# Performance work log

Hardware: AMD Instinct MI355X
Metric: run time of the kernel (lower is better)

The kernel has to match this reference:

```python
import jax, jax.numpy as jnp
import numpy as np

B, W, L, J, I, O = 512, 1024, 64, 8, 32, 128


def setup_inputs() -> dict:
    key = jax.random.key(0)
    ks = jax.random.split(key, 9)
    wm = jax.random.normal(ks[0], (B, W, L), dtype=jnp.float32)
    constants = jax.random.uniform(ks[1], (J, L), minval=-1.0, maxval=1.0, dtype=jnp.float32)
    gammas = jax.random.uniform(ks[2], (J, L), minval=0.0, maxval=1.0, dtype=jnp.float32)
    body_w = jax.random.normal(ks[3], (J, I, L), dtype=jnp.float32) / np.sqrt(L).astype(np.float32)
    body_b = jax.random.normal(ks[4], (J, I), dtype=jnp.float32) * 0.01
    slot_w = jax.random.normal(ks[5], (J, L * I, L), dtype=jnp.float32) / np.sqrt(L).astype(np.float32)
    slot_b = jax.random.normal(ks[6], (J, L * I), dtype=jnp.float32) * 0.01
    head_w = jax.random.normal(ks[7], (O, I), dtype=jnp.float32) / np.sqrt(I).astype(np.float32)
    head_b = jax.random.normal(ks[8], (O,), dtype=jnp.float32) * 0.01
    return {"working_memory": wm, "constants": constants, "gammas": gammas,
            "body_w": body_w, "body_b": body_b, "slot_w": slot_w, "slot_b": slot_b,
            "head_w": head_w, "head_b": head_b}


def reference(working_memory, constants, gammas, body_w, body_b, slot_w, slot_b, head_w, head_b):
    temperature = 1.0
    g = jnp.clip(gammas, 0.0, 1.0)            # (J,L), torch.clamp equivalent
    w1 = 1.0 - g                               # per-element weight (1-gamma)
    # match_scores[j,b,w] = sum_l w1[j,l] * (c[j,l] - wm[b,w,l])^2, expanded to
    # avoid materializing a (J,B,W,L) intermediate:
    A = jnp.sum(w1 * constants * constants, axis=1)                      # (J,)
    cross = jnp.einsum('jl,bwl->jbw', w1 * constants, working_memory)    # (J,B,W)
    quad = jnp.einsum('jl,bwl->jbw', w1, working_memory * working_memory)
    scores = A[:, None, None] - 2.0 * cross + quad                       # (J,B,W)
    attn = jax.nn.softmax(-scores / temperature, axis=-1)                # (J,B,W)
    best = jnp.einsum('jbw,bwl->jbl', attn, working_memory)              # (J,B,L)
    total_mq = jnp.sum(attn * scores, axis=-1).sum(axis=0)               # (B,)
    # body: per-premise Linear(L->I), scaled by mean clamped gamma
    captured = jnp.einsum('jbl,jil->jbi', best, body_w) + body_b[:, None, :]
    g_avg = g.mean(axis=1)                                               # (J,)
    captured_vars = jnp.einsum('j,jbi->bi', g_avg, captured)             # (B,I)
    # slot selector: per-premise Linear(L -> L*I), softmax over slots,
    # scatter best_props values into slots (the original inner l-loop).
    slot_logits = jnp.einsum('jbl,jkl->jbk', best, slot_w) + slot_b[:, None, :]
    slot_probs = jax.nn.softmax(slot_logits.reshape(J, -1, L, I), axis=-1)
    captured_vars = captured_vars + jnp.einsum('jbli,jbl->bi', slot_probs, best)
    output = captured_vars @ head_w.T + head_b                           # (B,O)
    confidence = jnp.exp(-total_mq)[:, None]                             # (B,1)
    return confidence * output
```

## Files before the change

### kernel.cpp

```cpp
#include <hip/hip_runtime.h>
#include <cstdint>
#include <cstddef>

#define B_ 512
#define W_ 1024
#define L_ 64
#define J_ 8
#define I_ 32
#define O_ 128


typedef const __attribute__((address_space(1))) void* gas_ptr;
typedef __attribute__((address_space(3))) void* las_ptr;

__global__ __launch_bounds__(64) void k0_prep(const float* __restrict__ constants,
    const float* __restrict__ gammas, float* __restrict__ wcg,
    float* __restrict__ w1g, float* __restrict__ Ag)
{
  const int l = threadIdx.x;
  #pragma unroll
  for (int j = 0; j < J_; ++j) {
    float g = gammas[j*L_ + l];
    g = fminf(fmaxf(g, 0.f), 1.f);
    float c = constants[j*L_ + l];
    float w1 = 1.f - g;
    w1g[j*L_ + l] = w1;
    wcg[j*L_ + l] = -2.f * w1 * c;
  }
  if (l < J_) {
    float a = 0.f;
    for (int c = 0; c < L_; ++c) {
      float g = gammas[l*L_ + c];
      g = fminf(fmaxf(g, 0.f), 1.f);
      float cc = constants[l*L_ + c];
      a += (1.f - g) * cc * cc;
    }
    Ag[l] = a;
  }
}

__global__ __launch_bounds__(256, 2) void k12_fused(const float* __restrict__ wm,
    const float* __restrict__ wcg, const float* __restrict__ w1g,
    const float* __restrict__ Ag, float* __restrict__ bpart, float* __restrict__ stats)
{
  __shared__ __align__(16) float xs[2][64 * 64];
  __shared__ __align__(16) float es[4][64 * 2];

  const int tid = threadIdx.x;
  const int b = blockIdx.x, h = blockIdx.y;
  const int lane = tid & 63;
  const int wvu = __builtin_amdgcn_readfirstlane(tid >> 6);
  const int j0  = wvu * 2;
  const int wm15 = lane & 15;
  const int cg = lane & 15, rs = lane >> 4;
  const int rl = lane >> 4, pcg = lane & 15;

  const float* wmb = wm + (size_t)b * (W_*L_) + (size_t)h * (512*L_);

  float acc0[4] = {0.f, 0.f, 0.f, 0.f};
  float acc1[4] = {0.f, 0.f, 0.f, 0.f};
  float esum[2] = {0.f, 0.f}, msum[2] = {0.f, 0.f}, m0v[2];

  auto stage = [&](const float* csrc, float* ldst) {
    #pragma unroll
    for (int k = 0; k < 4; ++k) {
      const int grow = wvu*16 + k*4 + rl;
      const int lcg  = pcg ^ (k*4 + rl);
      __builtin_amdgcn_global_load_lds(
          (gas_ptr)(csrc + grow*64 + lcg*4),
          (las_ptr)(ldst + (wvu*16 + k*4)*64), 16, 0, 0);
    }
  };

  stage(wmb, &xs[0][0]);
  asm volatile("s_waitcnt vmcnt(0)" ::: "memory");
  __builtin_amdgcn_s_barrier();

  for (int ch = 0; ch < 8; ++ch) {
    float* xb = &xs[ch & 1][0];

    if (ch < 7)
      stage(wmb + (ch+1) * (64*L_), &xs[(ch+1) & 1][0]);

    float a10 = 0.f, a11 = 0.f, a20 = 0.f, a21 = 0.f;
    #pragma unroll
    for (int c = 0; c < 16; ++c) {
      const int col = c ^ wm15;
      float4 x = *(const float4*)&xb[lane*64 + col*4];
      float4 xq;
      xq.x = x.x*x.x; xq.y = x.y*x.y; xq.z = x.z*x.z; xq.w = x.w*x.w;
      float4 wc0 = *(const float4*)(wcg + (j0  )*L_ + c*4);
      float4 wc1 = *(const float4*)(wcg + (j0+1)*L_ + c*4);
      float4 w10 = *(const float4*)(w1g + (j0  )*L_ + c*4);
      float4 w11 = *(const float4*)(w1g + (j0+1)*L_ + c*4);
      a10 = fmaf(wc0.x, x.x, a10); a10 = fmaf(wc0.y, x.y, a10);
      a10 = fmaf(wc0.z, x.z, a10); a10 = fmaf(wc0.w, x.w, a10);
      a11 = fmaf(wc1.x, x.x, a11); a11 = fmaf(wc1.y, x.y, a11);
      a11 = fmaf(wc1.z, x.z, a11); a11 = fmaf(wc1.w, x.w, a11);
      a20 = fmaf(w10.x, xq.x, a20); a20 = fmaf(w10.y, xq.y, a20);
      a20 = fmaf(w10.z, xq.z, a20); a20 = fmaf(w10.w, xq.w, a20);
      a21 = fmaf(w11.x, xq.x, a21); a21 = fmaf(w11.y, xq.y, a21);
      a21 = fmaf(w11.w, xq.w, a21); a21 = fmaf(w11.z, xq.z, a21);
    }
    float s0v = Ag[j0]   + a10 + a20;
    float s1v = Ag[j0+1] + a11 + a21;

    if (ch == 0) {
      float mn0 = s0v, mn1 = s1v;
      #pragma unroll
      for (int off = 1; off < 64; off <<= 1) {
        mn0 = fminf(mn0, __shfl_xor(mn0, off));
        mn1 = fminf(mn1, __shfl_xor(mn1, off));
      }
      m0v[0] = mn0; m0v[1] = mn1;
    }

    float e0 = __expf(m0v[0] - s0v);
    float e1 = __expf(m0v[1] - s1v);
    esum[0] += e0; msum[0] = fmaf(e0, s0v, msum[0]);
    esum[1] += e1; msum[1] = fmaf(e1, s1v, msum[1]);
    *(float2*)&es[wvu][lane*2] = make_float2(e0, e1);

    asm volatile("s_waitcnt lgkmcnt(0)" ::: "memory");

    #pragma unroll
    for (int it = 0; it < 16; it += 2) {
      const int w0 = rs*16 + it;
      float4 e4 = *(const float4*)&es[wvu][w0*2];
      float4 xA = *(const float4*)&xb[w0*64     + (cg ^ ( w0    & 15))*4];
      float4 xB = *(const float4*)&xb[(w0+1)*64 + (cg ^ ((w0+1) & 15))*4];
      acc0[0] = fmaf(e4.x, xA.x, acc0[0]); acc0[1] = fmaf(e4.x, xA.y, acc0[1]);
      acc0[2] = fmaf(e4.x, xA.z, acc0[2]); acc0[3] = fmaf(e4.x, xA.w, acc0[3]);
      acc1[0] = fmaf(e4.y, xA.x, acc1[0]); acc1[1] = fmaf(e4.y, xA.y, acc1[1]);
      acc1[2] = fmaf(e4.y, xA.z, acc1[2]); acc1[3] = fmaf(e4.y, xA.w, acc1[3]);
      acc0[0] = fmaf(e4.z, xB.x, acc0[0]); acc0[1] = fmaf(e4.z, xB.y, acc0[1]);
      acc0[2] = fmaf(e4.z, xB.z, acc0[2]); acc0[3] = fmaf(e4.z, xB.w, acc0[3]);
      acc1[0] = fmaf(e4.w, xB.x, acc1[0]); acc1[1] = fmaf(e4.w, xB.y, acc1[1]);
      acc1[2] = fmaf(e4.w, xB.z, acc1[2]); acc1[3] = fmaf(e4.w, xB.w, acc1[3]);
    }

    if (ch < 7) {
      asm volatile("s_waitcnt vmcnt(0) lgkmcnt(0)" ::: "memory");
      __builtin_amdgcn_s_barrier();
    }
  }

  #pragma unroll
  for (int u = 0; u < 2; ++u) {
    float e = esum[u], m = msum[u];
    #pragma unroll
    for (int off = 1; off < 64; off <<= 1) {
      e += __shfl_xor(e, off);
      m += __shfl_xor(m, off);
    }
    if (lane == 0) {
      float* st = stats + (((size_t)h*B_ + b)*J_ + (j0+u))*4;
      st[0] = m0v[u]; st[1] = e; st[2] = m;
    }
  }

  #pragma unroll
  for (int q = 0; q < 4; ++q) {
    acc0[q] += __shfl_xor(acc0[q], 16);
    acc0[q] += __shfl_xor(acc0[q], 32);
    acc1[q] += __shfl_xor(acc1[q], 16);
    acc1[q] += __shfl_xor(acc1[q], 32);
  }
  if (lane < 16) {
    float* bp0 = &bpart[(((size_t)h*J_ + j0    )*B_ + b)*L_ + cg*4];
    float* bp1 = &bpart[(((size_t)h*J_ + j0 + 1)*B_ + b)*L_ + cg*4];
    *(float4*)bp0 = make_float4(acc0[0], acc0[1], acc0[2], acc0[3]);
    *(float4*)bp1 = make_float4(acc1[0], acc1[1], acc1[2], acc1[3]);
  }
}

__global__ __launch_bounds__(128) void k2b_combine(const float* __restrict__ bpart,
    const float* __restrict__ stats, float* __restrict__ best, float* __restrict__ conf)
{
  __shared__ float mred[J_];
  const int b = blockIdx.x, tid = threadIdx.x;
  const int j = tid >> 4, q = tid & 15;
  const float* st0 = stats + ((size_t)b*J_ + j)*4;
  const float* st1 = stats + (((size_t)B_ + b)*J_ + j)*4;
  float m0a = st0[0], E0 = st0[1], M0 = st0[2];
  float m0b = st1[0], E1 = st1[1], M1 = st1[2];
  float M = fminf(m0a, m0b);
  float s0 = __expf(M - m0a), s1 = __expf(M - m0b);
  float E = s0*E0 + s1*E1;
  float inv = 1.f / E;
  float4 p0 = *(const float4*)&bpart[((size_t)j*B_ + b)*L_ + q*4];
  float4 p1 = *(const float4*)&bpart[(((size_t)J_ + j)*B_ + b)*L_ + q*4];
  float4 o;
  o.x = (s0*p0.x + s1*p1.x) * inv;
  o.y = (s0*p0.y + s1*p1.y) * inv;
  o.z = (s0*p0.z + s1*p1.z) * inv;
  o.w = (s0*p0.w + s1*p1.w) * inv;
  *(float4*)&best[((size_t)j*B_ + b)*L_ + q*4] = o;
  if (q == 0) mred[j] = (s0*M0 + s1*M1) * inv;
  __syncthreads();
  if (tid == 0) {
    float mq = 0.f;
    #pragma unroll
    for (int jj = 0; jj < J_; ++jj) mq += mred[jj];
    conf[b] = __expf(-mq);
  }
}

__global__ __launch_bounds__(256) void k3_slot(const float* __restrict__ slot_w,
    const float* __restrict__ slot_b, const float* __restrict__ best,
    float* __restrict__ partial)
{
  const int bx = blockIdx.y;
  const int j = bx >> 3, lg = bx & 7;
  const int bc = blockIdx.x;
  const int tid = threadIdx.x;
  const int wv = tid >> 6, lane = tid & 63;
  const int l2 = lane >> 5, i = lane & 31;
  const int l = lg*8 + wv*2 + l2;
  const int r = l*I_ + i;

  const float* swr = slot_w + ((size_t)j*(L_*I_) + r) * L_;
  float sw[L_];
  #pragma unroll
  for (int c = 0; c < 16; ++c) {
    float4 t = ((const float4*)swr)[c];
    sw[c*4+0] = t.x; sw[c*4+1] = t.y; sw[c*4+2] = t.z; sw[c*4+3] = t.w;
  }
  const float sb = slot_b[j*(L_*I_) + r];
  const float* bestj = best + (size_t)j * B_ * L_;
  float* pout = partial + (size_t)bx * (B_*I_);
  const int lidx = lg*8 + wv*2;

  for (int bi = 0; bi < 32; bi += 4) {
    const int b0 = bc*32 + bi;
    const float* bw[4];
    #pragma unroll
    for (int u = 0; u < 4; ++u) bw[u] = bestj + (size_t)(b0+u) * L_;
    float pa[4], pb[4];
    #pragma unroll
    for (int u = 0; u < 4; ++u) { pa[u] = sb; pb[u] = 0.f; }
    #pragma unroll
    for (int c = 0; c < L_; c += 2) {
      #pragma unroll
      for (int u = 0; u < 4; ++u) {
        pa[u] = fmaf(bw[u][c+0], sw[c+0], pa[u]);
        pb[u] = fmaf(bw[u][c+1], sw[c+1], pb[u]);
      }
    }
    float e[4], sm[4];
    #pragma unroll
    for (int u = 0; u < 4; ++u) { e[u] = __expf(pa[u] + pb[u]); sm[u] = e[u]; }
    #pragma unroll
    for (int mask = 16; mask; mask >>= 1)
      #pragma unroll
      for (int u = 0; u < 4; ++u) sm[u] += __shfl_xor(sm[u], mask);
    float cv[4];
    #pragma unroll
    for (int u = 0; u < 4; ++u) {
      float bv = l2 ? bw[u][lidx+1] : bw[u][lidx];
      cv[u] = (e[u] / sm[u]) * bv;
    }
    #pragma unroll
    for (int u = 0; u < 4; ++u) cv[u] += __shfl_xor(cv[u], 32);
    if (l2 == 0) {
      #pragma unroll
      for (int u = 0; u < 4; ++u)
        pout[(size_t)(b0+u)*I_ + i] = cv[u];
    }
  }
}

__global__ __launch_bounds__(128) void k4_head(const float* __restrict__ partial,
    const float* __restrict__ best, const float* __restrict__ gammas,
    const float* __restrict__ body_w, const float* __restrict__ body_b,
    const float* __restrict__ head_w, const float* __restrict__ head_b,
    const float* __restrict__ conf, float* __restrict__ out)
{
  __shared__ float gavg[J_];
  __shared__ float cvred[4][I_];
  __shared__ float cvf[I_];
  const int b = blockIdx.x, tid = threadIdx.x;
  const int i = tid & 31, q = tid >> 5;
  if (tid < J_) {
    float gsum = 0.f;
    for (int l = 0; l < L_; ++l) {
      float g = gammas[tid*L_ + l];
      gsum += fminf(fmaxf(g, 0.f), 1.f);
    }
    gavg[tid] = gsum * (1.f / L_);
  }
  __syncthreads();

  float acc = 0.f;
  for (int s = q; s < 64; s += 4)
    acc += partial[((size_t)s*B_ + b)*I_ + i];

  #pragma unroll
  for (int u = 0; u < 2; ++u) {
    const int j = q + u*4;
    const float* bwv  = best + ((size_t)j*B_ + b)*L_;
    const float* wrow = body_w + (size_t)(j*I_ + i)*L_;
    float d0 = body_b[j*I_ + i], d1 = 0.f, d2 = 0.f, d3 = 0.f;
    #pragma unroll
    for (int c = 0; c < L_; c += 4) {
      d0 = fmaf(bwv[c+0], wrow[c+0], d0);
      d1 = fmaf(bwv[c+1], wrow[c+1], d1);
      d2 = fmaf(bwv[c+2], wrow[c+2], d2);
      d3 = fmaf(bwv[c+3], wrow[c+3], d3);
    }
    acc = fmaf(gavg[j], (d0 + d1) + (d2 + d3), acc);
  }
  cvred[q][i] = acc;
  __syncthreads();
  if (tid < I_)
    cvf[i] = cvred[0][i] + cvred[1][i] + cvred[2][i] + cvred[3][i];
  __syncthreads();
  float oacc = head_b[tid];
  #pragma unroll
  for (int i2 = 0; i2 < I_; ++i2) oacc = fmaf(cvf[i2], head_w[tid*I_ + i2], oacc);
  out[(size_t)b*O_ + tid] = conf[b] * oacc;
}

extern "C" void kernel_launch(void* const* d_in, const int* in_sizes, int n_in,
                              void* d_out, int out_size, void* d_ws, size_t ws_size,
                              hipStream_t stream) {
  const float* wm        = (const float*)d_in[0];
  const float* constants = (const float*)d_in[1];
  const float* gammas    = (const float*)d_in[2];
  const float* body_w    = (const float*)d_in[3];
  const float* body_b    = (const float*)d_in[4];
  const float* slot_w    = (const float*)d_in[5];
  const float* slot_b    = (const float*)d_in[6];
  const float* head_w    = (const float*)d_in[7];
  const float* head_b    = (const float*)d_in[8];
  float* out = (float*)d_out;

  float* ws      = (float*)d_ws;
  float* wcg     = ws;
  float* w1g     = wcg + J_*L_;
  float* Ag      = w1g + J_*L_;
  float* best    = Ag + 16;
  float* conf    = best + (size_t)J_*B_*L_;
  float* partial = conf + B_;
  float* bpart   = partial + (size_t)64*B_*I_;
  float* stats   = bpart + (size_t)2*J_*B_*L_;

  hipLaunchKernelGGL(k0_prep, dim3(1), dim3(64), 0, stream,
                     constants, gammas, wcg, w1g, Ag);
  hipLaunchKernelGGL(k12_fused, dim3(B_, 2), dim3(256), 0, stream,
                     wm, wcg, w1g, Ag, bpart, stats);
  hipLaunchKernelGGL(k2b_combine, dim3(B_), dim3(128), 0, stream,
                     bpart, stats, best, conf);
  hipLaunchKernelGGL(k3_slot, dim3(16, 64), dim3(256), 0, stream,
                     slot_w, slot_b, best, partial);
  hipLaunchKernelGGL(k4_head, dim3(B_), dim3(128), 0, stream,
                     partial, best, gammas, body_w, body_b, head_w, head_b, conf, out);
}
```

Measured before the change: 282.9 us.

## Split attention W dimension into eight blocks, combine partial softmax results

The fused score/attention kernel now launches 8 blocks per batch row instead of 2. Each block handles one 64-row chunk of working memory, so the in-block double-buffered chunk loop goes away. The combine kernel merges 8 partial (min, expsum, weighted-sum) statistics and partial best vectors with rescaling. This aims to raise parallelism and hide load latency by running many blocks at once rather than software pipelining. The cost is more partial-output traffic and a heavier combine step.

```diff
diff --git a/kernel.cpp b/kernel.cpp
--- a/kernel.cpp
+++ b/kernel.cpp
@@ -8,6 +8,7 @@
 #define J_ 8
 #define I_ 32
 #define O_ 128
+#define H_ 8
 
 
 typedef const __attribute__((address_space(1))) void* gas_ptr;
@@ -43,7 +44,7 @@
     const float* __restrict__ wcg, const float* __restrict__ w1g,
     const float* __restrict__ Ag, float* __restrict__ bpart, float* __restrict__ stats)
 {
-  __shared__ __align__(16) float xs[2][64 * 64];
+  __shared__ __align__(16) float xs[64 * 64];
   __shared__ __align__(16) float es[4][64 * 2];
 
   const int tid = threadIdx.x;
@@ -55,107 +56,86 @@
   const int cg = lane & 15, rs = lane >> 4;
   const int rl = lane >> 4, pcg = lane & 15;
 
-  const float* wmb = wm + (size_t)b * (W_*L_) + (size_t)h * (512*L_);
+  const float* wmb = wm + (size_t)b * (W_*L_) + (size_t)h * (64*L_);
+
+  #pragma unroll
+  for (int k = 0; k < 4; ++k) {
+    const int grow = wvu*16 + k*4 + rl;
+    const int lcg  = pcg ^ (k*4 + rl);
+    __builtin_amdgcn_global_load_lds(
+        (gas_ptr)(wmb + grow*64 + lcg*4),
+        (las_ptr)&xs[(wvu*16 + k*4)*64], 16, 0, 0);
+  }
+  asm volatile("s_waitcnt vmcnt(0)" ::: "memory");
+  __builtin_amdgcn_s_barrier();
+
+  float a10 = 0.f, a11 = 0.f, a20 = 0.f, a21 = 0.f;
+  #pragma unroll
+  for (int c = 0; c < 16; ++c) {
+    const int col = c ^ wm15;
+    float4 x = *(const float4*)&xs[lane*64 + col*4];
+    float4 xq;
+    xq.x = x.x*x.x; xq.y = x.y*x.y; xq.z = x.z*x.z; xq.w = x.w*x.w;
+    float4 wc0 = *(const float4*)(wcg + (j0  )*L_ + c*4);
+    float4 wc1 = *(const float4*)(wcg + (j0+1)*L_ + c*4);
+    float4 w10 = *(const float4*)(w1g + (j0  )*L_ + c*4);
+    float4 w11 = *(const float4*)(w1g + (j0+1)*L_ + c*4);
+    a10 = fmaf(wc0.x, x.x, a10); a10 = fmaf(wc0.y, x.y, a10);
+    a10 = fmaf(wc0.z, x.z, a10); a10 = fmaf(wc0.w, x.w, a10);
+    a11 = fmaf(wc1.x, x.x, a11); a11 = fmaf(wc1.y, x.y, a11);
+    a11 = fmaf(wc1.z, x.z, a11); a11 = fmaf(wc1.w, x.w, a11);
+    a20 = fmaf(w10.x, xq.x, a20); a20 = fmaf(w10.y, xq.y, a20);
+    a20 = fmaf(w10.z, xq.z, a20); a20 = fmaf(w10.w, xq.w, a20);
+    a21 = fmaf(w11.x, xq.x, a21); a21 = fmaf(w11.y, xq.y, a21);
+    a21 = fmaf(w11.z, xq.z, a21); a21 = fmaf(w11.w, xq.w, a21);
+  }
+  float s0v = Ag[j0]   + a10 + a20;
+  float s1v = Ag[j0+1] + a11 + a21;
+
+  float mn0 = s0v, mn1 = s1v;
+  #pragma unroll
+  for (int off = 1; off < 64; off <<= 1) {
+    mn0 = fminf(mn0, __shfl_xor(mn0, off));
+    mn1 = fminf(mn1, __shfl_xor(mn1, off));
+  }
+
+  float e0 = __expf(mn0 - s0v);
+  float e1 = __expf(mn1 - s1v);
+  float esum0 = e0, esum1 = e1;
+  float msum0 = e0 * s0v, msum1 = e1 * s1v;
+  *(float2*)&es[wvu][lane*2] = make_float2(e0, e1);
+  asm volatile("s_waitcnt lgkmcnt(0)" ::: "memory");
 
   float acc0[4] = {0.f, 0.f, 0.f, 0.f};
   float acc1[4] = {0.f, 0.f, 0.f, 0.f};
-  float esum[2] = {0.f, 0.f}, msum[2] = {0.f, 0.f}, m0v[2];
-
-  auto stage = [&](const float* csrc, float* ldst) {
-    #pragma unroll
-    for (int k = 0; k < 4; ++k) {
-      const int grow = wvu*16 + k*4 + rl;
-      const int lcg  = pcg ^ (k*4 + rl);
-      __builtin_amdgcn_global_load_lds(
-          (gas_ptr)(csrc + grow*64 + lcg*4),
-          (las_ptr)(ldst + (wvu*16 + k*4)*64), 16, 0, 0);
-    }
-  };
-
-  stage(wmb, &xs[0][0]);
-  asm volatile("s_waitcnt vmcnt(0)" ::: "memory");
-  __builtin_amdgcn_s_barrier();
-
-  for (int ch = 0; ch < 8; ++ch) {
-    float* xb = &xs[ch & 1][0];
-
-    if (ch < 7)
-      stage(wmb + (ch+1) * (64*L_), &xs[(ch+1) & 1][0]);
-
-    float a10 = 0.f, a11 = 0.f, a20 = 0.f, a21 = 0.f;
-    #pragma unroll
-    for (int c = 0; c < 16; ++c) {
-      const int col = c ^ wm15;
-      float4 x = *(const float4*)&xb[lane*64 + col*4];
-      float4 xq;
-      xq.x = x.x*x.x; xq.y = x.y*x.y; xq.z = x.z*x.z; xq.w = x.w*x.w;
-      float4 wc0 = *(const float4*)(wcg + (j0  )*L_ + c*4);
-      float4 wc1 = *(const float4*)(wcg + (j0+1)*L_ + c*4);
-      float4 w10 = *(const float4*)(w1g + (j0  )*L_ + c*4);
-      float4 w11 = *(const float4*)(w1g + (j0+1)*L_ + c*4);
-      a10 = fmaf(wc0.x, x.x, a10); a10 = fmaf(wc0.y, x.y, a10);
-      a10 = fmaf(wc0.z, x.z, a10); a10 = fmaf(wc0.w, x.w, a10);
-      a11 = fmaf(wc1.x, x.x, a11); a11 = fmaf(wc1.y, x.y, a11);
-      a11 = fmaf(wc1.z, x.z, a11); a11 = fmaf(wc1.w, x.w, a11);
-      a20 = fmaf(w10.x, xq.x, a20); a20 = fmaf(w10.y, xq.y, a20);
-      a20 = fmaf(w10.z, xq.z, a20); a20 = fmaf(w10.w, xq.w, a20);
-      a21 = fmaf(w11.x, xq.x, a21); a21 = fmaf(w11.y, xq.y, a21);
-      a21 = fmaf(w11.w, xq.w, a21); a21 = fmaf(w11.z, xq.z, a21);
-    }
-    float s0v = Ag[j0]   + a10 + a20;
-    float s1v = Ag[j0+1] + a11 + a21;
-
-    if (ch == 0) {
-      float mn0 = s0v, mn1 = s1v;
-      #pragma unroll
-      for (int off = 1; off < 64; off <<= 1) {
-        mn0 = fminf(mn0, __shfl_xor(mn0, off));
-        mn1 = fminf(mn1, __shfl_xor(mn1, off));
-      }
-      m0v[0] = mn0; m0v[1] = mn1;
-    }
-
-    float e0 = __expf(m0v[0] - s0v);
-    float e1 = __expf(m0v[1] - s1v);
-    esum[0] += e0; msum[0] = fmaf(e0, s0v, msum[0]);
-    esum[1] += e1; msum[1] = fmaf(e1, s1v, msum[1]);
-    *(float2*)&es[wvu][lane*2] = make_float2(e0, e1);
-
-    asm volatile("s_waitcnt lgkmcnt(0)" ::: "memory");
-
-    #pragma unroll
-    for (int it = 0; it < 16; it += 2) {
-      const int w0 = rs*16 + it;
-      float4 e4 = *(const float4*)&es[wvu][w0*2];
-      float4 xA = *(const float4*)&xb[w0*64     + (cg ^ ( w0    & 15))*4];
-      float4 xB = *(const float4*)&xb[(w0+1)*64 + (cg ^ ((w0+1) & 15))*4];
-      acc0[0] = fmaf(e4.x, xA.x, acc0[0]); acc0[1] = fmaf(e4.x, xA.y, acc0[1]);
-      acc0[2] = fmaf(e4.x, xA.z, acc0[2]); acc0[3] = fmaf(e4.x, xA.w, acc0[3]);
-      acc1[0] = fmaf(e4.y, xA.x, acc1[0]); acc1[1] = fmaf(e4.y, xA.y, acc1[1]);
-      acc1[2] = fmaf(e4.y, xA.z, acc1[2]); acc1[3] = fmaf(e4.y, xA.w, acc1[3]);
-      acc0[0] = fmaf(e4.z, xB.x, acc0[0]); acc0[1] = fmaf(e4.z, xB.y, acc0[1]);
-      acc0[2] = fmaf(e4.z, xB.z, acc0[2]); acc0[3] = fmaf(e4.z, xB.w, acc0[3]);
-      acc1[0] = fmaf(e4.w, xB.x, acc1[0]); acc1[1] = fmaf(e4.w, xB.y, acc1[1]);
-      acc1[2] = fmaf(e4.w, xB.z, acc1[2]); acc1[3] = fmaf(e4.w, xB.w, acc1[3]);
-    }
-
-    if (ch < 7) {
-      asm volatile("s_waitcnt vmcnt(0) lgkmcnt(0)" ::: "memory");
-      __builtin_amdgcn_s_barrier();
-    }
-  }
-
-  #pragma unroll
-  for (int u = 0; u < 2; ++u) {
-    float e = esum[u], m = msum[u];
+  #pragma unroll
+  for (int it = 0; it < 16; it += 2) {
+    const int w0 = rs*16 + it;
+    float4 e4 = *(const float4*)&es[wvu][w0*2];
+    float4 xA = *(const float4*)&xs[w0*64     + (cg ^ ( w0    & 15))*4];
+    float4 xB = *(const float4*)&xs[(w0+1)*64 + (cg ^ ((w0+1) & 15))*4];
+    acc0[0] = fmaf(e4.x, xA.x, acc0[0]); acc0[1] = fmaf(e4.x, xA.y, acc0[1]);
+    acc0[2] = fmaf(e4.x, xA.z, acc0[2]); acc0[3] = fmaf(e4.x, xA.w, acc0[3]);
+    acc1[0] = fmaf(e4.y, xA.x, acc1[0]); acc1[1] = fmaf(e4.y, xA.y, acc1[1]);
+    acc1[2] = fmaf(e4.y, xA.z, acc1[2]); acc1[3] = fmaf(e4.y, xA.w, acc1[3]);
+    acc0[0] = fmaf(e4.z, xB.x, acc0[0]); acc0[1] = fmaf(e4.z, xB.y, acc0[1]);
+    acc0[2] = fmaf(e4.z, xB.z, acc0[2]); acc0[3] = fmaf(e4.z, xB.w, acc0[3]);
+    acc1[0] = fmaf(e4.w, xB.x, acc1[0]); acc1[1] = fmaf(e4.w, xB.y, acc1[1]);
+    acc1[2] = fmaf(e4.w, xB.z, acc1[2]); acc1[3] = fmaf(e4.w, xB.w, acc1[3]);
+  }
+
+  {
+    float ea = esum0, ma = msum0, eb = esum1, mb = msum1;
     #pragma unroll
     for (int off = 1; off < 64; off <<= 1) {
-      e += __shfl_xor(e, off);
-      m += __shfl_xor(m, off);
+      ea += __shfl_xor(ea, off); ma += __shfl_xor(ma, off);
+      eb += __shfl_xor(eb, off); mb += __shfl_xor(mb, off);
     }
     if (lane == 0) {
-      float* st = stats + (((size_t)h*B_ + b)*J_ + (j0+u))*4;
-      st[0] = m0v[u]; st[1] = e; st[2] = m;
+      float* st0 = stats + (((size_t)h*B_ + b)*J_ + j0)*4;
+      st0[0] = mn0; st0[1] = ea; st0[2] = ma;
+      float* st1 = stats + (((size_t)h*B_ + b)*J_ + j0 + 1)*4;
+      st1[0] = mn1; st1[1] = eb; st1[2] = mb;
     }
   }
 
@@ -180,23 +160,34 @@
   __shared__ float mred[J_];
   const int b = blockIdx.x, tid = threadIdx.x;
   const int j = tid >> 4, q = tid & 15;
-  const float* st0 = stats + ((size_t)b*J_ + j)*4;
-  const float* st1 = stats + (((size_t)B_ + b)*J_ + j)*4;
-  float m0a = st0[0], E0 = st0[1], M0 = st0[2];
-  float m0b = st1[0], E1 = st1[1], M1 = st1[2];
-  float M = fminf(m0a, m0b);
-  float s0 = __expf(M - m0a), s1 = __expf(M - m0b);
-  float E = s0*E0 + s1*E1;
-  float inv = 1.f / E;
-  float4 p0 = *(const float4*)&bpart[((size_t)j*B_ + b)*L_ + q*4];
-  float4 p1 = *(const float4*)&bpart[(((size_t)J_ + j)*B_ + b)*L_ + q*4];
-  float4 o;
-  o.x = (s0*p0.x + s1*p1.x) * inv;
-  o.y = (s0*p0.y + s1*p1.y) * inv;
-  o.z = (s0*p0.z + s1*p1.z) * inv;
-  o.w = (s0*p0.w + s1*p1.w) * inv;
+
+  float m0[H_], E[H_], Mq[H_];
+  #pragma unroll
+  for (int u = 0; u < H_; ++u) {
+    const float* st = stats + (((size_t)u*B_ + b)*J_ + j)*4;
+    m0[u] = st[0]; E[u] = st[1]; Mq[u] = st[2];
+  }
+  float M = m0[0];
+  #pragma unroll
+  for (int u = 1; u < H_; ++u) M = fminf(M, m0[u]);
+  float s[H_], Esum = 0.f, Msum = 0.f;
+  #pragma unroll
+  for (int u = 0; u < H_; ++u) {
+    s[u] = __expf(M - m0[u]);
+    Esum = fmaf(s[u], E[u], Esum);
+    Msum = fmaf(s[u], Mq[u], Msum);
+  }
+  float inv = 1.f / Esum;
+  float4 o = make_float4(0.f, 0.f, 0.f, 0.f);
+  #pragma unroll
+  for (int u = 0; u < H_; ++u) {
+    float4 p = *(const float4*)&bpart[(((size_t)u*J_ + j)*B_ + b)*L_ + q*4];
+    o.x = fmaf(s[u], p.x, o.x); o.y = fmaf(s[u], p.y, o.y);
+    o.z = fmaf(s[u], p.z, o.z); o.w = fmaf(s[u], p.w, o.w);
+  }
+  o.x *= inv; o.y *= inv; o.z *= inv; o.w *= inv;
   *(float4*)&best[((size_t)j*B_ + b)*L_ + q*4] = o;
-  if (q == 0) mred[j] = (s0*M0 + s1*M1) * inv;
+  if (q == 0) mred[j] = Msum * inv;
   __syncthreads();
   if (tid == 0) {
     float mq = 0.f;
@@ -343,11 +334,11 @@
   float* conf    = best + (size_t)J_*B_*L_;
   float* partial = conf + B_;
   float* bpart   = partial + (size_t)64*B_*I_;
-  float* stats   = bpart + (size_t)2*J_*B_*L_;
+  float* stats   = bpart + (size_t)H_*J_*B_*L_;
 
   hipLaunchKernelGGL(k0_prep, dim3(1), dim3(64), 0, stream,
                      constants, gammas, wcg, w1g, Ag);
-  hipLaunchKernelGGL(k12_fused, dim3(B_, 2), dim3(256), 0, stream,
+  hipLaunchKernelGGL(k12_fused, dim3(B_, H_), dim3(256), 0, stream,
                      wm, wcg, w1g, Ag, bpart, stats);
   hipLaunchKernelGGL(k2b_combine, dim3(B_), dim3(128), 0, stream,
                      bpart, stats, best, conf);
```

After: 256.4 us. -9.4%, faster.
